# Optimization experiments

Measured on AMD Instinct MI355X. Metric: run time of the kernel, lower is better.

The kernel has to match this reference:

```python
import jax, jax.numpy as jnp
import numpy as np

EPS = 1e-8  # torch F.cosine_similarity default eps


def setup_inputs() -> dict:
    key = jax.random.key(0)
    k1, k2, k3 = jax.random.split(key, 3)
    B, C, H2, W2 = 2, 512, 128, 128  # B must be 2 (broadcast in match_prototypes)
    s_features = jax.random.normal(k1, (B, C, H2, W2), dtype=jnp.float32)
    q_features = jax.random.normal(k2, (B, C, H2, W2), dtype=jnp.float32)
    # block-constant 0/1 masks at image resolution (512x512), 32x32 blocks
    base = jax.random.randint(k3, (B, 1, 16, 16), 0, 2).astype(jnp.float32)
    s_masks = jnp.repeat(jnp.repeat(base, 32, axis=2), 32, axis=3)  # (B,1,512,512)
    return {"s_features": s_features, "s_masks": s_masks, "q_features": q_features}


def _compute_prototypes(features, masks):
    # features: (B,C,H,W), masks: (B,1,H,W). Torch: (feat*mask).sum((2,3))/mask.sum((2,3))
    protos = []
    for c in range(2):
        m = (masks == c).astype(features.dtype)
        protos.append((features * m).sum(axis=(2, 3)) / m.sum(axis=(2, 3)))
    return jnp.stack(protos)  # (2,B,C)


def _match_prototypes(q_features, prototypes):
    # Faithful to torch broadcast: q (B,1,C,HW) vs prototypes (2,B,C,1); requires B==2.
    B, C, H, W = q_features.shape
    q = q_features.reshape(B, C, H * W)
    # num[i,j,s] = sum_c q[i,c,s] * prototypes[i,j,c]  (avoids (2,2,C,HW) intermediate)
    num = jnp.einsum('ics,ijc->ijs', q, prototypes)
    qn = jnp.linalg.norm(q, axis=1)            # (B,HW)
    pn = jnp.linalg.norm(prototypes, axis=2)   # (2,B)
    sim = num / jnp.maximum(qn[:, None, :] * pn[:, :, None], EPS)  # (2,B,HW)
    q_logits = jnp.argmax(sim, axis=1).reshape(B, H, W)
    return q_logits, sim


def reference(s_features, s_masks, q_features):
    B, C, H2, W2 = s_features.shape
    # F.interpolate(..., mode='bilinear', align_corners=False) == half-pixel linear, no antialias
    s_masks_r = jax.image.resize(s_masks, (s_masks.shape[0], 1, H2, W2),
                                 method='linear', antialias=False)
    prototypes = _compute_prototypes(s_features, s_masks_r)  # (2,B,C)
    q_out4, sim = _match_prototypes(q_features, prototypes)
    # original also returns decode(q_features) logits; backbone is external, omitted
    return (q_out4, sim, prototypes)
```

## Files before the change

kernel.cpp:

```cpp
#include <hip/hip_runtime.h>
#include <math.h>

#define HW 16384
#define NC 512

#define WS_SUMALL 0
#define WS_SUM1   1024
#define WS_PART   2048

#define OUT_SIM   32768
#define OUT_PROTO 98304


__global__ __launch_bounds__(256) void k_sums(const float* __restrict__ feat,
                                              const float* __restrict__ masks,
                                              float* __restrict__ ws) {
  const int blk = blockIdx.x;
  const int b = blk >> 9;
  const int tid = threadIdx.x;
  __shared__ float cell[256];
  cell[tid] = masks[(size_t)b * 262144 + (size_t)(tid >> 4) * 16384 + (size_t)(tid & 15) * 32];
  __syncthreads();
  const float4* f = (const float4*)(feat + (size_t)blk * HW);
  float aall = 0.0f, a1 = 0.0f;
  #pragma unroll
  for (int k = 0; k < 16; ++k) {
    const int idx = tid + k * 256;
    const float4 v = f[idx];
    const float m = cell[((idx >> 8) << 4) | ((idx >> 1) & 15)];
    const float s4 = (v.x + v.y) + (v.z + v.w);
    aall += s4;
    a1 = fmaf(m, s4, a1);
  }
  #pragma unroll
  for (int mm = 32; mm >= 1; mm >>= 1) {
    aall += __shfl_xor(aall, mm);
    a1 += __shfl_xor(a1, mm);
  }
  __shared__ float s0[4], s1[4];
  const int w = tid >> 6, lane = tid & 63;
  if (lane == 0) { s0[w] = aall; s1[w] = a1; }
  __syncthreads();
  if (tid == 0) {
    ws[WS_SUMALL + blk] = (s0[0] + s0[1]) + (s0[2] + s0[3]);
    ws[WS_SUM1 + blk] = (s1[0] + s1[1]) + (s1[2] + s1[3]);
  }
}

__global__ __launch_bounds__(256) void k_dot(const float* __restrict__ q,
                                             const float* __restrict__ masks,
                                             float* __restrict__ ws) {
  const int bid = blockIdx.x;
  const int b = bid >> 8;
  const int pt = (bid >> 2) & 63;
  const int qd = bid & 3;
  const int tid = threadIdx.x;
  const int w = tid >> 6, lane = tid & 63;

  __shared__ float P[2][128];
  __shared__ float red0[4], red1[4];
  __shared__ float4 S[4][3][64];

  {
    const size_t off = (size_t)(tid >> 4) * 16384 + (size_t)(tid & 15) * 32;
    const int c0 = __popcll(__ballot(masks[off] > 0.5f));
    const int c1 = __popcll(__ballot(masks[262144 + off] > 0.5f));
    if (lane == 0) { red0[w] = (float)c0; red1[w] = (float)c1; }
  }
  __syncthreads();
  const float n1j[2] = {64.0f * ((red0[0] + red0[1]) + (red0[2] + red0[3])),
                        64.0f * ((red1[0] + red1[1]) + (red1[2] + red1[3]))};

  const int cbase = qd * 128;
  {
    const int j = tid >> 7, cl = tid & 127;
    const float sall = ws[WS_SUMALL + j * 512 + cbase + cl];
    const float sv1 = ws[WS_SUM1 + j * 512 + cbase + cl];
    P[j][cl] = b ? (sv1 / n1j[j]) : ((sall - sv1) / (16384.0f - n1j[j]));
  }
  __syncthreads();

  const int ss0 = pt * 256;
  const float* qb = q + (size_t)(b * NC + cbase + w * 32) * HW + ss0 + 4 * lane;
  float4 n0 = {0.f, 0.f, 0.f, 0.f}, n1 = {0.f, 0.f, 0.f, 0.f}, qq = {0.f, 0.f, 0.f, 0.f};
  #pragma unroll 8
  for (int cc = 0; cc < 32; ++cc) {
    const float4 v = *(const float4*)(qb + (size_t)cc * HW);
    const float p0 = P[0][w * 32 + cc], p1 = P[1][w * 32 + cc];
    n0.x = fmaf(v.x, p0, n0.x); n0.y = fmaf(v.y, p0, n0.y);
    n0.z = fmaf(v.z, p0, n0.z); n0.w = fmaf(v.w, p0, n0.w);
    n1.x = fmaf(v.x, p1, n1.x); n1.y = fmaf(v.y, p1, n1.y);
    n1.z = fmaf(v.z, p1, n1.z); n1.w = fmaf(v.w, p1, n1.w);
    qq.x = fmaf(v.x, v.x, qq.x); qq.y = fmaf(v.y, v.y, qq.y);
    qq.z = fmaf(v.z, v.z, qq.z); qq.w = fmaf(v.w, v.w, qq.w);
  }
  S[w][0][lane] = n0; S[w][1][lane] = n1; S[w][2][lane] = qq;
  __syncthreads();

  {
    const float* Sf = (const float*)S;
    const int px = tid;
    const size_t base = WS_PART + (size_t)(((b * 64 + pt) * 4 + qd) * 3) * 256 + px;
    #pragma unroll
    for (int comp = 0; comp < 3; ++comp) {
      const float acc = (Sf[(0 * 3 + comp) * 256 + px] + Sf[(1 * 3 + comp) * 256 + px]) +
                        (Sf[(2 * 3 + comp) * 256 + px] + Sf[(3 * 3 + comp) * 256 + px]);
      ws[base + (size_t)comp * 256] = acc;
    }
  }
}

__global__ __launch_bounds__(256) void k_final(const float* __restrict__ masks,
                                               const float* __restrict__ ws,
                                               float* __restrict__ out) {
  const int b = blockIdx.x >> 6;
  const int pt = blockIdx.x & 63;
  const int tid = threadIdx.x;
  const int w = tid >> 6, lane = tid & 63;
  __shared__ float red0[4], red1[4], nrm[8];

  {
    const size_t off = (size_t)(tid >> 4) * 16384 + (size_t)(tid & 15) * 32;
    const int c0 = __popcll(__ballot(masks[off] > 0.5f));
    const int c1 = __popcll(__ballot(masks[262144 + off] > 0.5f));
    if (lane == 0) { red0[w] = (float)c0; red1[w] = (float)c1; }
  }
  __syncthreads();
  const float n1j[2] = {64.0f * ((red0[0] + red0[1]) + (red0[2] + red0[3])),
                        64.0f * ((red1[0] + red1[1]) + (red1[2] + red1[3]))};

  float a0 = 0.0f, a1 = 0.0f;
  #pragma unroll
  for (int t = 0; t < 2; ++t) {
    const int ch = tid + t * 256;
    #pragma unroll
    for (int j = 0; j < 2; ++j) {
      const float sall = ws[WS_SUMALL + j * 512 + ch];
      const float sv1 = ws[WS_SUM1 + j * 512 + ch];
      const float val = b ? (sv1 / n1j[j]) : ((sall - sv1) / (16384.0f - n1j[j]));
      if (pt == 0) out[OUT_PROTO + b * 1024 + j * 512 + ch] = val;
      if (j == 0) a0 = fmaf(val, val, a0); else a1 = fmaf(val, val, a1);
    }
  }
  #pragma unroll
  for (int mm = 32; mm >= 1; mm >>= 1) {
    a0 += __shfl_xor(a0, mm);
    a1 += __shfl_xor(a1, mm);
  }
  if (lane == 0) { nrm[w] = a0; nrm[4 + w] = a1; }
  __syncthreads();
  const float pn0 = sqrtf((nrm[0] + nrm[1]) + (nrm[2] + nrm[3]));
  const float pn1 = sqrtf((nrm[4] + nrm[5]) + (nrm[6] + nrm[7]));

  const int px = tid;
  const float* base = ws + WS_PART + (size_t)((b * 64 + pt) * 4) * 3 * 256 + px;
  float fn0 = 0.0f, fn1 = 0.0f, fqq = 0.0f;
  #pragma unroll
  for (int qd = 0; qd < 4; ++qd) {
    fn0 += base[(qd * 3 + 0) * 256];
    fn1 += base[(qd * 3 + 1) * 256];
    fqq += base[(qd * 3 + 2) * 256];
  }
  const float qn = sqrtf(fqq);
  const float sim0 = fn0 / fmaxf(qn * pn0, 1e-8f);
  const float sim1 = fn1 / fmaxf(qn * pn1, 1e-8f);
  const int ss = pt * 256 + px;
  out[OUT_SIM + (b * 2 + 0) * HW + ss] = sim0;
  out[OUT_SIM + (b * 2 + 1) * HW + ss] = sim1;
  out[b * HW + ss] = (sim1 > sim0) ? 1.0f : 0.0f;
}

extern "C" void kernel_launch(void* const* d_in, const int* in_sizes, int n_in,
                              void* d_out, int out_size, void* d_ws, size_t ws_size,
                              hipStream_t stream) {
  const float* s_features = (const float*)d_in[0];
  const float* s_masks = (const float*)d_in[1];
  const float* q_features = (const float*)d_in[2];
  float* out = (float*)d_out;
  float* ws = (float*)d_ws;

  hipLaunchKernelGGL(k_sums, dim3(1024), dim3(256), 0, stream, s_features, s_masks, ws);
  hipLaunchKernelGGL(k_dot, dim3(512), dim3(256), 0, stream, q_features, s_masks, ws);
  hipLaunchKernelGGL(k_final, dim3(128), dim3(256), 0, stream, s_masks, ws, out);
}
```

Before: 154.6 us.

## Fuse final similarity kernel into dot kernel via last-block atomic counter

Removes the separate k_final launch. Each group of four k_dot blocks that share a pixel tile bumps an atomic counter, and the last block to arrive reduces the partial sums and writes the similarities, argmax and prototypes. The counters are zeroed inside k_sums. This saves one kernel launch and its gap, at the cost of threadfence and atomic overhead and some serial tail work in the finishing blocks.

```diff
diff --git a/kernel.cpp b/kernel.cpp
--- a/kernel.cpp
+++ b/kernel.cpp
@@ -6,7 +6,8 @@
 
 #define WS_SUMALL 0
 #define WS_SUM1   1024
-#define WS_PART   2048
+#define WS_CNT    2048
+#define WS_PART   2304
 
 #define OUT_SIM   32768
 #define OUT_PROTO 98304
@@ -18,6 +19,7 @@
   const int blk = blockIdx.x;
   const int b = blk >> 9;
   const int tid = threadIdx.x;
+  if (blk < 128 && tid == 0) ((unsigned int*)ws)[WS_CNT + blk] = 0u;
   __shared__ float cell[256];
   cell[tid] = masks[(size_t)b * 262144 + (size_t)(tid >> 4) * 16384 + (size_t)(tid & 15) * 32];
   __syncthreads();
@@ -49,7 +51,8 @@
 
 __global__ __launch_bounds__(256) void k_dot(const float* __restrict__ q,
                                              const float* __restrict__ masks,
-                                             float* __restrict__ ws) {
+                                             float* __restrict__ ws,
+                                             float* __restrict__ out) {
   const int bid = blockIdx.x;
   const int b = bid >> 8;
   const int pt = (bid >> 2) & 63;
@@ -60,6 +63,7 @@
   __shared__ float P[2][128];
   __shared__ float red0[4], red1[4];
   __shared__ float4 S[4][3][64];
+  __shared__ int lastflag;
 
   {
     const size_t off = (size_t)(tid >> 4) * 16384 + (size_t)(tid & 15) * 32;
@@ -76,7 +80,9 @@
     const int j = tid >> 7, cl = tid & 127;
     const float sall = ws[WS_SUMALL + j * 512 + cbase + cl];
     const float sv1 = ws[WS_SUM1 + j * 512 + cbase + cl];
-    P[j][cl] = b ? (sv1 / n1j[j]) : ((sall - sv1) / (16384.0f - n1j[j]));
+    const float val = b ? (sv1 / n1j[j]) : ((sall - sv1) / (16384.0f - n1j[j]));
+    P[j][cl] = val;
+    if (pt == 0) out[OUT_PROTO + b * 1024 + j * 512 + cbase + cl] = val;
   }
   __syncthreads();
 
@@ -108,27 +114,18 @@
       ws[base + (size_t)comp * 256] = acc;
     }
   }
-}
 
-__global__ __launch_bounds__(256) void k_final(const float* __restrict__ masks,
-                                               const float* __restrict__ ws,
-                                               float* __restrict__ out) {
-  const int b = blockIdx.x >> 6;
-  const int pt = blockIdx.x & 63;
-  const int tid = threadIdx.x;
-  const int w = tid >> 6, lane = tid & 63;
-  __shared__ float red0[4], red1[4], nrm[8];
-
-  {
-    const size_t off = (size_t)(tid >> 4) * 16384 + (size_t)(tid & 15) * 32;
-    const int c0 = __popcll(__ballot(masks[off] > 0.5f));
-    const int c1 = __popcll(__ballot(masks[262144 + off] > 0.5f));
-    if (lane == 0) { red0[w] = (float)c0; red1[w] = (float)c1; }
+  __threadfence();
+  __syncthreads();
+  if (tid == 0) {
+    const unsigned int old = atomicAdd((unsigned int*)ws + WS_CNT + b * 64 + pt, 1u);
+    lastflag = (old == 3u) ? 1 : 0;
   }
   __syncthreads();
-  const float n1j[2] = {64.0f * ((red0[0] + red0[1]) + (red0[2] + red0[3])),
-                        64.0f * ((red1[0] + red1[1]) + (red1[2] + red1[3]))};
+  if (!lastflag) return;
+  __threadfence();
 
+  __shared__ float nrm[8];
   float a0 = 0.0f, a1 = 0.0f;
   #pragma unroll
   for (int t = 0; t < 2; ++t) {
@@ -138,7 +135,6 @@
       const float sall = ws[WS_SUMALL + j * 512 + ch];
       const float sv1 = ws[WS_SUM1 + j * 512 + ch];
       const float val = b ? (sv1 / n1j[j]) : ((sall - sv1) / (16384.0f - n1j[j]));
-      if (pt == 0) out[OUT_PROTO + b * 1024 + j * 512 + ch] = val;
       if (j == 0) a0 = fmaf(val, val, a0); else a1 = fmaf(val, val, a1);
     }
   }
@@ -153,13 +149,13 @@
   const float pn1 = sqrtf((nrm[4] + nrm[5]) + (nrm[6] + nrm[7]));
 
   const int px = tid;
-  const float* base = ws + WS_PART + (size_t)((b * 64 + pt) * 4) * 3 * 256 + px;
+  const float* pbase = ws + WS_PART + (size_t)((b * 64 + pt) * 4) * 3 * 256 + px;
   float fn0 = 0.0f, fn1 = 0.0f, fqq = 0.0f;
   #pragma unroll
-  for (int qd = 0; qd < 4; ++qd) {
-    fn0 += base[(qd * 3 + 0) * 256];
-    fn1 += base[(qd * 3 + 1) * 256];
-    fqq += base[(qd * 3 + 2) * 256];
+  for (int q4 = 0; q4 < 4; ++q4) {
+    fn0 += pbase[(q4 * 3 + 0) * 256];
+    fn1 += pbase[(q4 * 3 + 1) * 256];
+    fqq += pbase[(q4 * 3 + 2) * 256];
   }
   const float qn = sqrtf(fqq);
   const float sim0 = fn0 / fmaxf(qn * pn0, 1e-8f);
@@ -180,6 +176,5 @@
   float* ws = (float*)d_ws;
 
   hipLaunchKernelGGL(k_sums, dim3(1024), dim3(256), 0, stream, s_features, s_masks, ws);
-  hipLaunchKernelGGL(k_dot, dim3(512), dim3(256), 0, stream, q_features, s_masks, ws);
-  hipLaunchKernelGGL(k_final, dim3(128), dim3(256), 0, stream, s_masks, ws, out);
+  hipLaunchKernelGGL(k_dot, dim3(512), dim3(256), 0, stream, q_features, s_masks, ws, out);
 }
```

Result: slower. 227.9 us (+47.5%).
